# Kernel tuning notes

Measured on AMD Instinct MI355X. Metric: run time of the kernel, lower is better.

Reference implementation:

```python
import jax, jax.numpy as jnp
import numpy as np

MAX_CACHE_LEN = 4096


def _rotate_half(t):
    d = t.shape[-1] // 2
    return jnp.concatenate([-t[..., d:], t[..., :d]], axis=-1)


def _apply_rope(t, cos, sin):
    # t: (B, S, H, D); cos/sin: (S, D)
    c = cos[None, :, None, :]
    s = sin[None, :, None, :]
    return t * c + _rotate_half(t) * s


def setup_inputs() -> dict:
    key = jax.random.key(0)
    ks = jax.random.split(key, 7)
    B, S, E, D, KVH = 1, 2048, 2048, 64, 8
    sc = 0.02
    x = jax.random.normal(ks[0], (B, S, E), dtype=jnp.float32)
    Wq = jax.random.normal(ks[1], (E, E), dtype=jnp.float32) * sc
    Wk = jax.random.normal(ks[2], (KVH * D, E), dtype=jnp.float32) * sc
    Wv = jax.random.normal(ks[3], (KVH * D, E), dtype=jnp.float32) * sc
    Wo = jax.random.normal(ks[4], (E, E), dtype=jnp.float32) * sc
    # RoPE tables
    pos = jnp.arange(S, dtype=jnp.float32)[:, None]
    inv_freq = 1.0 / (10000.0 ** (jnp.arange(0, D, 2, dtype=jnp.float32) / D))
    ang = pos * inv_freq[None, :]              # (S, D/2)
    ang = jnp.concatenate([ang, ang], axis=-1)  # (S, D)
    cos = jnp.cos(ang)
    sin = jnp.sin(ang)
    # additive causal mask (1,1,S,S): 0 where allowed, -1e9 where masked
    causal = jnp.tril(jnp.ones((S, S), dtype=bool))
    attn_mask = jnp.where(causal, 0.0, -1e9).astype(jnp.float32)[None, None]
    return {"x": x, "Wq": Wq, "Wk": Wk, "Wv": Wv, "Wo": Wo,
            "cos": cos, "sin": sin, "attn_mask": attn_mask, "last_pos": S}


def reference(x, Wq, Wk, Wv, Wo, cos, sin, attn_mask, last_pos):
    B, S, E = x.shape
    D = cos.shape[-1]
    H = E // D
    KVH = Wk.shape[0] // D
    group = H // KVH

    q = (x @ Wq.T).reshape(B, S, H, D)
    k = (x @ Wk.T).reshape(B, S, KVH, D)
    v = (x @ Wv.T).reshape(B, S, KVH, D)

    q = _apply_rope(q, cos, sin)
    k = _apply_rope(k, cos, sin)

    # KV-cache write (index_copy at positions [last_pos-S, last_pos)), then slice [:last_pos]
    key_cache = jnp.zeros((B, MAX_CACHE_LEN, KVH, D), dtype=x.dtype)
    value_cache = jnp.zeros((B, MAX_CACHE_LEN, KVH, D), dtype=x.dtype)
    key_cache = jax.lax.dynamic_update_slice(key_cache, jax.lax.stop_gradient(k), (0, last_pos - S, 0, 0))
    value_cache = jax.lax.dynamic_update_slice(value_cache, jax.lax.stop_gradient(v), (0, last_pos - S, 0, 0))
    kc = key_cache[:, :last_pos]    # (B, T, KVH, D)
    vc = value_cache[:, :last_pos]

    # GQA: repeat kv heads to match q heads
    kc = jnp.repeat(kc, group, axis=2)  # (B, T, H, D)
    vc = jnp.repeat(vc, group, axis=2)

    scale = 1.0 / np.sqrt(D)
    scores = jnp.einsum('bqhd,bkhd->bhqk', q, kc) * scale
    scores = scores + attn_mask
    probs = jax.nn.softmax(scores.astype(jnp.float32), axis=-1).astype(x.dtype)
    attn = jnp.einsum('bhqk,bkhd->bqhd', probs, vc)  # (B, S, H, D)
    out = attn.reshape(B, S, E) @ Wo.T
    return out
```

## Files before the change

kernel.cpp:

```cpp
#include <hip/hip_runtime.h>
#include <stdint.h>

typedef unsigned short u16;
typedef unsigned int   u32;

typedef __bf16 bf16x8 __attribute__((ext_vector_type(8)));
typedef float  fx4    __attribute__((ext_vector_type(4)));
typedef u16    u16x8  __attribute__((ext_vector_type(8)));
typedef u16    u16x4  __attribute__((ext_vector_type(4)));

typedef __attribute__((address_space(1))) unsigned int as1_u32;
typedef __attribute__((address_space(3))) unsigned int as3_u32;

__device__ __forceinline__ void gload_lds16(const void* g, void* lds) {
  __builtin_amdgcn_global_load_lds((const as1_u32*)(uintptr_t)g,
                                   (as3_u32*)(uintptr_t)lds, 16, 0, 0);
}

__device__ __forceinline__ float b2f(u32 bits) {
  union { u32 i; float f; } v; v.i = bits << 16; return v.f;
}
__device__ __forceinline__ u16 f2b(float f) {
  union { float f; u32 i; } v; v.f = f;
  u32 x = v.i;
  return (u16)((x + 0x7fffu + ((x >> 16) & 1u)) >> 16);
}

__global__ __launch_bounds__(256) void cast_kernel(
    const float* __restrict__ s0, const float* __restrict__ s1,
    const float* __restrict__ s2, const float* __restrict__ s3,
    const float* __restrict__ s4, u16* __restrict__ dst)
{
  const size_t i8 = ((size_t)blockIdx.x * 256 + threadIdx.x) * 8;
  if (i8 >= 14680064) return;
  const float* src; size_t off;
  if      (i8 <  4194304) { src = s0; off = i8; }
  else if (i8 <  8388608) { src = s1; off = i8 - 4194304; }
  else if (i8 <  9437184) { src = s2; off = i8 - 8388608; }
  else if (i8 < 10485760) { src = s3; off = i8 - 9437184; }
  else                    { src = s4; off = i8 - 10485760; }
  const float4 a = *(const float4*)(src + off);
  const float4 b = *(const float4*)(src + off + 4);
  u16x8 o;
  o[0] = f2b(a.x); o[1] = f2b(a.y); o[2] = f2b(a.z); o[3] = f2b(a.w);
  o[4] = f2b(b.x); o[5] = f2b(b.y); o[6] = f2b(b.z); o[7] = f2b(b.w);
  *(u16x8*)(dst + i8) = o;
}

template <int MODE>
__global__ __launch_bounds__(256) void gemm_bt(
    const u16* __restrict__ A, const u16* __restrict__ B0,
    const u16* __restrict__ B1, const u16* __restrict__ B2,
    void* __restrict__ Cv, int K, int split1, int split2, int ldc,
    const float* __restrict__ cosb, const float* __restrict__ sinb,
    u16* __restrict__ vtg)
{
  __shared__ __align__(16) u16 smem[3 * 8192];

  const int n0 = blockIdx.x * 128;
  const int m0 = blockIdx.y * 128;

  const u16* Bsel; int nb;
  if (n0 < split1)      { Bsel = B0; nb = n0; }
  else if (n0 < split2) { Bsel = B1; nb = n0 - split1; }
  else                  { Bsel = B2; nb = n0 - split2; }

  const int tid  = threadIdx.x;
  const int wave = tid >> 6, lane = tid & 63;
  const int wm = wave >> 1, wn = wave & 1;
  const int quad = lane >> 4, l16 = lane & 15;

  fx4 acc[4][4];
#pragma unroll
  for (int i = 0; i < 4; ++i)
#pragma unroll
    for (int j = 0; j < 4; ++j) acc[i][j] = fx4{0.f, 0.f, 0.f, 0.f};

  const int row = tid >> 2;
  const int cc  = (tid & 3) * 8;
  auto stage = [&](int kt, int b) {
    u16* As = smem + b * 8192;
    u16* Bs = As + 4096;
    const int k0 = kt * 32;
#pragma unroll
    for (int i = 0; i < 2; ++i) {
      const int r2 = row + i * 64;
      const int s  = tid + i * 256;
      gload_lds16(A    + (size_t)(m0 + r2) * K + k0 + cc, As + s * 8);
      gload_lds16(Bsel + (size_t)(nb + r2) * K + k0 + cc, Bs + s * 8);
    }
  };

  const int KT = K >> 5;
  stage(0, 0);
  stage(1, 1);

  int cur = 0, nxt2 = 2;
#pragma unroll 1
  for (int kt = 0; kt < KT; ++kt) {
    if (kt < KT - 1) asm volatile("s_waitcnt vmcnt(4)\n\ts_barrier" ::: "memory");
    else             asm volatile("s_waitcnt vmcnt(0)\n\ts_barrier" ::: "memory");
    if (kt + 2 < KT) {
      stage(kt + 2, nxt2);
      nxt2 = (nxt2 == 2) ? 0 : nxt2 + 1;
    }

    const u16* As = smem + cur * 8192;
    const u16* Bs = As + 4096;
    cur = (cur == 2) ? 0 : cur + 1;

    bf16x8 af[4], bfr[4];
#pragma unroll
    for (int t = 0; t < 4; ++t) {
      af[t]  = *(const bf16x8*)&As[(wm * 64 + t * 16 + l16) * 32 + quad * 8];
      bfr[t] = *(const bf16x8*)&Bs[(wn * 64 + t * 16 + l16) * 32 + quad * 8];
    }
#pragma unroll
    for (int ti = 0; ti < 4; ++ti)
#pragma unroll
      for (int tj = 0; tj < 4; ++tj)
        acc[ti][tj] = __builtin_amdgcn_mfma_f32_16x16x32_bf16(
            af[ti], bfr[tj], acc[ti][tj], 0, 0, 0);
  }

  if (MODE == 1) {
    float* C = (float*)Cv;
#pragma unroll
    for (int ti = 0; ti < 4; ++ti) {
      const int row_b = m0 + wm * 64 + ti * 16 + quad * 4;
#pragma unroll
      for (int tj = 0; tj < 4; ++tj) {
        const int col = n0 + wn * 64 + tj * 16 + l16;
#pragma unroll
        for (int r = 0; r < 4; ++r)
          C[(size_t)(row_b + r) * ldc + col] = acc[ti][tj][r];
      }
    }
  } else {
    u16* C = (u16*)Cv;
    const int cb = n0 + wn * 64;
    if (cb < 2560) {
      const float qs = (cb < 2048) ? 0.125f : 1.0f;
#pragma unroll
      for (int ti = 0; ti < 4; ++ti) {
#pragma unroll
        for (int r = 0; r < 4; ++r) {
          const int s = m0 + wm * 64 + ti * 16 + quad * 4 + r;
          const float* cr = cosb + s * 64;
          const float* sr = sinb + s * 64;
          u16* orow = C + (size_t)s * 3072 + cb;
#pragma unroll
          for (int tj = 0; tj < 2; ++tj) {
            const int d0 = tj * 16 + l16, d1 = d0 + 32;
            const float x0 = acc[ti][tj][r], x1 = acc[ti][tj + 2][r];
            orow[d0] = f2b((x0 * cr[d0] - x1 * sr[d0]) * qs);
            orow[d1] = f2b((x1 * cr[d1] + x0 * sr[d1]) * qs);
          }
        }
      }
    } else {
      const int vr0 = cb - 2560;
#pragma unroll
      for (int ti = 0; ti < 4; ++ti) {
        const int s0 = m0 + wm * 64 + ti * 16 + quad * 4;
#pragma unroll
        for (int tj = 0; tj < 4; ++tj) {
          const int vr = vr0 + tj * 16 + l16;
          u16x4 o;
#pragma unroll
          for (int r = 0; r < 4; ++r) o[r] = f2b(acc[ti][tj][r]);
          *(u16x4*)(vtg + (size_t)vr * 2048 + s0) = o;
        }
      }
    }
  }
}

__global__ __launch_bounds__(256) void attn_kernel(
    const u16* __restrict__ qkv, const u16* __restrict__ vt,
    u16* __restrict__ attnbuf)
{
  const int h   = blockIdx.y;
  const int kvh = h >> 2;
  const int tid = threadIdx.x;
  const int w = tid >> 6, lane = tid & 63;
  const int quad = lane >> 4, l16 = lane & 15;

  __shared__ __align__(16) u16 Qs[64][72];
  __shared__ __align__(16) u16 Ks[128][72];
  __shared__ __align__(16) u16 Vh[2][64][72];
  __shared__ __align__(16) u16 Ps[4][16][72];

  const int kcol = 2048 + kvh * 64;

#pragma unroll 1
  for (int pass = 0; pass < 2; ++pass) {
    const int bx = pass ? (31 - blockIdx.x) : blockIdx.x;
    const int r0 = bx * 64;
    const int nhalf  = bx + 1;
    const int ntiles = (bx + 2) >> 1;

    __syncthreads();

#pragma unroll
    for (int i = 0; i < 2; ++i) {
      const int idx = tid + i * 256;
      const int r = idx >> 3, dc = (idx & 7) * 8;
      *(uint4*)&Qs[r][dc] =
          *(const uint4*)(qkv + (size_t)(r0 + r) * 3072 + h * 64 + dc);
    }

    fx4 O[4];
    float l_r[4];
#pragma unroll
    for (int c = 0; c < 4; ++c) O[c] = fx4{0.f, 0.f, 0.f, 0.f};
#pragma unroll
    for (int r = 0; r < 4; ++r) l_r[r] = 0.f;

#pragma unroll 1
    for (int kt = 0; kt < ntiles; ++kt) {
      const int k0 = kt * 128;
      __syncthreads();
#pragma unroll
      for (int i = 0; i < 4; ++i) {
        const int idx = tid + i * 256;
        const int j = idx >> 3, dc = (idx & 7) * 8;
        *(uint4*)&Ks[j][dc] =
            *(const uint4*)(qkv + (size_t)(k0 + j) * 3072 + kcol + dc);
      }
#pragma unroll
      for (int i = 0; i < 4; ++i) {
        const int idx = tid + i * 256;
        const int hh = idx >> 9, rem = idx & 511;
        const int j = rem >> 3, dc = (rem & 7) * 8;
        *(uint4*)&Vh[hh][j][dc] =
            *(const uint4*)(vt + (size_t)(kvh * 64 + j) * 2048 + k0 + hh * 64 + dc);
      }
      __syncthreads();

      const bf16x8 aq0 = *(const bf16x8*)&Qs[w * 16 + l16][quad * 8];
      const bf16x8 aq1 = *(const bf16x8*)&Qs[w * 16 + l16][32 + quad * 8];

#pragma unroll
      for (int hh = 0; hh < 2; ++hh) {
        const int half = kt * 2 + hh;
        if (half < nhalf) {
          const int k0h = k0 + hh * 64;

          fx4 sc[4];
#pragma unroll
          for (int c = 0; c < 4; ++c) {
            const bf16x8 b0 = *(const bf16x8*)&Ks[hh * 64 + c * 16 + l16][quad * 8];
            const bf16x8 b1 = *(const bf16x8*)&Ks[hh * 64 + c * 16 + l16][32 + quad * 8];
            fx4 z = fx4{0.f, 0.f, 0.f, 0.f};
            z     = __builtin_amdgcn_mfma_f32_16x16x32_bf16(aq0, b0, z, 0, 0, 0);
            sc[c] = __builtin_amdgcn_mfma_f32_16x16x32_bf16(aq1, b1, z, 0, 0, 0);
          }

          const bool diag = (k0h >= r0);
#pragma unroll
          for (int c = 0; c < 4; ++c) {
#pragma unroll
            for (int r = 0; r < 4; ++r) {
              float p = __expf(sc[c][r]);
              if (diag && (k0h + c * 16 + l16 > r0 + w * 16 + quad * 4 + r)) p = 0.f;
              l_r[r] += p;
              Ps[w][quad * 4 + r][c * 16 + l16] = f2b(p);
            }
          }

          const bf16x8 ap0 = *(const bf16x8*)&Ps[w][l16][quad * 8];
          const bf16x8 ap1 = *(const bf16x8*)&Ps[w][l16][32 + quad * 8];
#pragma unroll
          for (int c = 0; c < 4; ++c) {
            const bf16x8 v0 = *(const bf16x8*)&Vh[hh][c * 16 + l16][quad * 8];
            const bf16x8 v1 = *(const bf16x8*)&Vh[hh][c * 16 + l16][32 + quad * 8];
            O[c] = __builtin_amdgcn_mfma_f32_16x16x32_bf16(ap0, v0, O[c], 0, 0, 0);
            O[c] = __builtin_amdgcn_mfma_f32_16x16x32_bf16(ap1, v1, O[c], 0, 0, 0);
          }
        }
      }
    }

#pragma unroll
    for (int r = 0; r < 4; ++r) {
      float l = l_r[r];
#pragma unroll
      for (int off = 1; off < 16; off <<= 1) l += __shfl_xor(l, off, 64);
      const float inv = 1.f / fmaxf(l, 1e-30f);
      const int qg = r0 + w * 16 + quad * 4 + r;
#pragma unroll
      for (int c = 0; c < 4; ++c)
        attnbuf[(size_t)qg * 2048 + h * 64 + c * 16 + l16] = f2b(O[c][r] * inv);
    }
  }
}

extern "C" void kernel_launch(void* const* d_in, const int* in_sizes, int n_in,
                              void* d_out, int out_size, void* d_ws, size_t ws_size,
                              hipStream_t stream) {
  const float* x    = (const float*)d_in[0];
  const float* Wq   = (const float*)d_in[1];
  const float* Wk   = (const float*)d_in[2];
  const float* Wv   = (const float*)d_in[3];
  const float* Wo   = (const float*)d_in[4];
  const float* cosb = (const float*)d_in[5];
  const float* sinb = (const float*)d_in[6];
  float* out = (float*)d_out;

  u16* ws      = (u16*)d_ws;
  u16* qkv     = ws;
  u16* attnbuf = ws + 6291456;
  u16* xb      = ws + 10485760;
  u16* Wqb     = ws + 14680064;
  u16* Wkb     = ws + 18874368;
  u16* Wvb     = ws + 19922944;
  u16* Wob     = ws + 20971520;
  u16* vtg     = ws + 25165824;

  cast_kernel<<<7168, 256, 0, stream>>>(x, Wq, Wk, Wv, Wo, xb);

  gemm_bt<0><<<dim3(24, 16), 256, 0, stream>>>(
      xb, Wqb, Wkb, Wvb, qkv, 2048, 2048, 2560, 3072, cosb, sinb, vtg);

  attn_kernel<<<dim3(16, 32), 256, 0, stream>>>(qkv, vtg, attnbuf);

  gemm_bt<1><<<dim3(16, 16), 256, 0, stream>>>(
      attnbuf, Wob, Wob, Wob, out, 2048, 1 << 30, 1 << 30, 2048, cosb, sinb, vtg);
}
```

Measured before the change: 231.3 us.

## Deepen GEMM LDS pipeline to four stages and specialize attention masking path

The GEMM kernel's shared-memory ring grows from three to four buffers, so three k-tiles are prefetched ahead. The vmcnt wait thresholds are adjusted to the remaining tile count, and buffer indexing becomes kt&3. This aims to hide more global-load latency, at the cost of more LDS per block and possibly lower occupancy. In the attention kernel, the causal-mask check is split into a diagonal branch and a mask-free branch. The software bf16 rounding is replaced with the hardware conversion, cutting per-element ALU work in the softmax stage.

```diff
diff --git a/kernel.cpp b/kernel.cpp
--- a/kernel.cpp
+++ b/kernel.cpp
@@ -24,6 +24,9 @@
   union { float f; u32 i; } v; v.f = f;
   u32 x = v.i;
   return (u16)((x + 0x7fffu + ((x >> 16) & 1u)) >> 16);
+}
+__device__ __forceinline__ u16 f2b_hw(float f) {
+  union { __bf16 b; u16 u; } v; v.b = (__bf16)f; return v.u;
 }
 
 __global__ __launch_bounds__(256) void cast_kernel(
@@ -55,7 +58,7 @@
     const float* __restrict__ cosb, const float* __restrict__ sinb,
     u16* __restrict__ vtg)
 {
-  __shared__ __align__(16) u16 smem[3 * 8192];
+  __shared__ __align__(16) u16 smem[4 * 8192];
 
   const int n0 = blockIdx.x * 128;
   const int m0 = blockIdx.y * 128;
@@ -78,8 +81,8 @@
 
   const int row = tid >> 2;
   const int cc  = (tid & 3) * 8;
-  auto stage = [&](int kt, int b) {
-    u16* As = smem + b * 8192;
+  auto stage = [&](int kt) {
+    u16* As = smem + (kt & 3) * 8192;
     u16* Bs = As + 4096;
     const int k0 = kt * 32;
 #pragma unroll
@@ -92,22 +95,19 @@
   };
 
   const int KT = K >> 5;
-  stage(0, 0);
-  stage(1, 1);
-
-  int cur = 0, nxt2 = 2;
+  stage(0); stage(1); stage(2);
+
 #pragma unroll 1
   for (int kt = 0; kt < KT; ++kt) {
-    if (kt < KT - 1) asm volatile("s_waitcnt vmcnt(4)\n\ts_barrier" ::: "memory");
-    else             asm volatile("s_waitcnt vmcnt(0)\n\ts_barrier" ::: "memory");
-    if (kt + 2 < KT) {
-      stage(kt + 2, nxt2);
-      nxt2 = (nxt2 == 2) ? 0 : nxt2 + 1;
-    }
-
-    const u16* As = smem + cur * 8192;
+    const int rem = KT - 1 - kt;
+    if (rem >= 3)      asm volatile("s_waitcnt vmcnt(12)\n\ts_barrier" ::: "memory");
+    else if (rem == 2) asm volatile("s_waitcnt vmcnt(8)\n\ts_barrier" ::: "memory");
+    else if (rem == 1) asm volatile("s_waitcnt vmcnt(4)\n\ts_barrier" ::: "memory");
+    else               asm volatile("s_waitcnt vmcnt(0)\n\ts_barrier" ::: "memory");
+    if (kt + 3 < KT) stage(kt + 3);
+
+    const u16* As = smem + (kt & 3) * 8192;
     const u16* Bs = As + 4096;
-    cur = (cur == 2) ? 0 : cur + 1;
 
     bf16x8 af[4], bfr[4];
 #pragma unroll
@@ -257,16 +257,25 @@
             sc[c] = __builtin_amdgcn_mfma_f32_16x16x32_bf16(aq1, b1, z, 0, 0, 0);
           }
 
-          const bool diag = (k0h >= r0);
-#pragma unroll
-          for (int c = 0; c < 4; ++c) {
-#pragma unroll
-            for (int r = 0; r < 4; ++r) {
-              float p = __expf(sc[c][r]);
-              if (diag && (k0h + c * 16 + l16 > r0 + w * 16 + quad * 4 + r)) p = 0.f;
-              l_r[r] += p;
-              Ps[w][quad * 4 + r][c * 16 + l16] = f2b(p);
-            }
+          if (k0h >= r0) {
+#pragma unroll
+            for (int c = 0; c < 4; ++c)
+#pragma unroll
+              for (int r = 0; r < 4; ++r) {
+                float p = __expf(sc[c][r]);
+                if (k0h + c * 16 + l16 > r0 + w * 16 + quad * 4 + r) p = 0.f;
+                l_r[r] += p;
+                Ps[w][quad * 4 + r][c * 16 + l16] = f2b_hw(p);
+              }
+          } else {
+#pragma unroll
+            for (int c = 0; c < 4; ++c)
+#pragma unroll
+              for (int r = 0; r < 4; ++r) {
+                const float p = __expf(sc[c][r]);
+                l_r[r] += p;
+                Ps[w][quad * 4 + r][c * 16 + l16] = f2b_hw(p);
+              }
           }
 
           const bf16x8 ap0 = *(const bf16x8*)&Ps[w][l16][quad * 8];
```

New measurement: 229.8 us. Within noise of the previous version (-0.7%).
